# Performance work log

Hardware: AMD Instinct MI355X
Metric: run time of the kernel (lower is better)

## Reference

```python
import jax, jax.numpy as jnp
import numpy as np

B, N, E, H = 8, 512, 1024, 128   # graphs, nodes, edges, hidden
T = 8                             # num_edge_types
HOPS = 3                          # graph_hops


def setup_inputs() -> dict:
    key = jax.random.key(0)
    ks = jax.random.split(key, 10)
    node_feature = jax.random.normal(ks[0], (B, N, H), dtype=jnp.float32)
    edge_vec = jax.random.randint(ks[1], (B, E), 0, T)  # per-edge type ids
    # sparse incidence matrices (one-hot edge endpoints), as the scipy .A densification does
    src = jax.random.randint(ks[2], (B, E), 0, N)
    tgt = jax.random.randint(ks[3], (B, E), 0, N)
    node2edge = jax.nn.one_hot(src, N, dtype=jnp.float32)                 # [B,E,N]
    edge2node = jnp.swapaxes(jax.nn.one_hot(tgt, N, dtype=jnp.float32), 1, 2)  # [B,N,E]
    s = 0.02  # xavier-ish init scale
    edge_weight_tensor = jax.random.normal(ks[4], (T, H * H), dtype=jnp.float32) * s
    Wz = jax.random.normal(ks[5], (2 * H, H), dtype=jnp.float32) * s
    Wr = jax.random.normal(ks[6], (2 * H, H), dtype=jnp.float32) * s
    Wt = jax.random.normal(ks[7], (2 * H, H), dtype=jnp.float32) * s
    Wf = jax.random.normal(ks[8], (4 * H, H), dtype=jnp.float32) * s
    bf = jnp.zeros((H,), dtype=jnp.float32)
    return {"node_feature": node_feature, "edge_vec": edge_vec,
            "node2edge": node2edge, "edge2node": edge2node,
            "edge_weight_tensor": edge_weight_tensor,
            "Wz": Wz, "Wr": Wr, "Wt": Wt, "Wf": Wf, "bf": bf}


def reference(node_feature, edge_vec, node2edge, edge2node,
              edge_weight_tensor, Wz, Wr, Wt, Wf, bf):
    Hd = node_feature.shape[-1]
    # gather per-edge weight matrices once (edge_vec is constant across hops)
    Wedge = edge_weight_tensor[edge_vec].reshape(edge_vec.shape + (Hd, Hd))  # [B,E,H,H]

    def mp(h, n2e, e2n):
        emb = jnp.einsum('ben,bnh->beh', n2e, h)          # gather node states to edges
        new = jnp.einsum('behd,bed->beh', Wedge, emb)     # per-edge-type matvec
        return jnp.einsum('bne,beh->bnh', e2n, new)       # scatter-aggregate to nodes

    def gru_step(h, a):
        x = jnp.concatenate([h, a], axis=-1)
        z = jax.nn.sigmoid(x @ Wz)
        r = jax.nn.sigmoid(x @ Wr)
        t = jnp.tanh(jnp.concatenate([r * h, a], axis=-1) @ Wt)
        return (1.0 - z) * h + z * t

    h = node_feature
    for _ in range(HOPS):
        bw = mp(h, node2edge, edge2node)
        fw = mp(h, jnp.swapaxes(edge2node, 1, 2), jnp.swapaxes(node2edge, 1, 2))
        # GatedFusion(fw, bw)
        z = jax.nn.sigmoid(jnp.concatenate([fw, bw, fw * bw, fw - bw], axis=-1) @ Wf + bf)
        agg = (1.0 - z) * fw + z * bw
        h = gru_step(h, agg)
    return h
```

## Files before the change

kernel.cpp:

```cpp
#include <hip/hip_runtime.h>

#define Bb 8
#define Nn 512
#define Ee 1024
#define Hh 128
#define Tt 8

__device__ __forceinline__ float sigm(float x){ return 1.0f/(1.0f + __expf(-x)); }
__device__ __forceinline__ float tanh_fast(float x){ return 2.0f/(1.0f + __expf(-2.0f*x)) - 1.0f; }

__device__ __forceinline__ void fma4(float* acc, float4 x, float4 w0, float4 w1, float4 w2, float4 w3){
  acc[0] += x.x*w0.x + x.y*w1.x + x.z*w2.x + x.w*w3.x;
  acc[1] += x.x*w0.y + x.y*w1.y + x.z*w2.y + x.w*w3.y;
  acc[2] += x.x*w0.z + x.y*w1.z + x.z*w2.z + x.w*w3.z;
  acc[3] += x.x*w0.w + x.y*w1.w + x.z*w2.w + x.w*w3.w;
}

__global__ void k_extract(const float4* __restrict__ n2e, const float4* __restrict__ e2n,
                          int* __restrict__ src, int* __restrict__ tgt){
  const int total1 = Bb*Ee*Nn/4;
  for (int i = blockIdx.x*blockDim.x + threadIdx.x; i < total1; i += gridDim.x*blockDim.x){
    float4 v = n2e[i];
    if (v.x!=0.f || v.y!=0.f || v.z!=0.f || v.w!=0.f){
      int base = i*4;
      int row = base >> 9;
      int n   = base & 511;
      if (v.x!=0.f) src[row] = n;
      if (v.y!=0.f) src[row] = n+1;
      if (v.z!=0.f) src[row] = n+2;
      if (v.w!=0.f) src[row] = n+3;
    }
  }
  const int total2 = Bb*Nn*Ee/4;
  for (int i = blockIdx.x*blockDim.x + threadIdx.x; i < total2; i += gridDim.x*blockDim.x){
    float4 v = e2n[i];
    if (v.x!=0.f || v.y!=0.f || v.z!=0.f || v.w!=0.f){
      int base = i*4;
      int row = base >> 10;
      int e   = base & 1023;
      int b = row >> 9, n = row & 511;
      int* tp = tgt + b*Ee;
      if (v.x!=0.f) tp[e]   = n;
      if (v.y!=0.f) tp[e+1] = n;
      if (v.z!=0.f) tp[e+2] = n;
      if (v.w!=0.f) tp[e+3] = n;
    }
  }
}

__global__ void k_transW(const float* __restrict__ W, float* __restrict__ WT){
  int i = blockIdx.x*blockDim.x + threadIdx.x;
  if (i >= Tt*Hh*Hh) return;
  int t = i >> 14;
  int h = (i >> 7) & 127;
  int d = i & 127;
  WT[(t*Hh + d)*Hh + h] = W[i];
}

__global__ void k_sort(const int* __restrict__ ev, int* __restrict__ order, int* __restrict__ offs){
  __shared__ int cnt[Tt], offs_s[Tt+1], pos[Tt];
  int b = blockIdx.x, tid = threadIdx.x;
  if (tid < Tt) cnt[tid] = 0;
  __syncthreads();
  for (int e = tid; e < Ee; e += blockDim.x) atomicAdd(&cnt[ev[b*Ee+e]], 1);
  __syncthreads();
  if (tid == 0){ offs_s[0]=0; for (int t=0;t<Tt;t++) offs_s[t+1]=offs_s[t]+cnt[t]; }
  __syncthreads();
  if (tid < Tt) pos[tid] = offs_s[tid];
  if (tid < Tt+1) offs[b*(Tt+1)+tid] = offs_s[tid];
  __syncthreads();
  for (int e = tid; e < Ee; e += blockDim.x){
    int t = ev[b*Ee+e];
    int p = atomicAdd(&pos[t], 1);
    order[b*Ee + p] = e;
  }
}

__global__ __launch_bounds__(256) void k_edge_mp(
    const float* __restrict__ h, const float* __restrict__ WT,
    const int* __restrict__ order, const int* __restrict__ offs,
    const int* __restrict__ src, const int* __restrict__ tgt,
    float* __restrict__ bw, float* __restrict__ fw)
{
  int x = blockIdx.x;
  int dir = x & 1;
  int bt  = x >> 1;
  int t = bt & 7, b = bt >> 3;
  int beg = offs[b*(Tt+1)+t], end = offs[b*(Tt+1)+t+1];
  int chunk0 = beg + blockIdx.y*32;
  if (chunk0 >= end) return;
  const int* gI = dir ? tgt : src;
  const int* sI = dir ? src : tgt;
  float* out = dir ? fw : bw;

  __shared__ float sEmb[32][Hh];
  __shared__ float sW[64][Hh];
  int tid = threadIdx.x;
  int te = tid >> 5, tc = tid & 31;
  int e0 = te*4, c0 = tc*4;
  const float* WTt = WT + t*Hh*Hh;

  for (int chunk = chunk0; chunk < end; chunk += gridDim.y*32){
    int ne = min(32, end - chunk);
    __syncthreads();
    for (int i = tid; i < 32*Hh; i += 256){
      int e = i >> 7, c = i & 127;
      float v = 0.f;
      if (e < ne){
        int eid = order[b*Ee + chunk + e];
        v = h[(b*Nn + gI[b*Ee + eid])*Hh + c];
      }
      sEmb[e][c] = v;
    }
    float acc[4][4] = {};
    for (int kc = 0; kc < Hh; kc += 64){
      __syncthreads();
      for (int i = tid; i < 64*Hh; i += 256){
        int d = i >> 7, c = i & 127;
        sW[d][c] = WTt[(kc + d)*Hh + c];
      }
      __syncthreads();
      #pragma unroll 4
      for (int k = 0; k < 64; k += 4){
        float4 evv[4], wv[4];
        #pragma unroll
        for (int j=0;j<4;j++) evv[j] = *(const float4*)&sEmb[e0+j][kc+k];
        #pragma unroll
        for (int j=0;j<4;j++) wv[j] = *(const float4*)&sW[k+j][c0];
        #pragma unroll
        for (int je=0;je<4;je++) fma4(acc[je], evv[je], wv[0], wv[1], wv[2], wv[3]);
      }
    }
    #pragma unroll
    for (int je=0;je<4;je++){
      int e = e0 + je;
      if (e < ne){
        int eid = order[b*Ee + chunk + e];
        int node = sI[b*Ee + eid];
        float* op = out + (size_t)(b*Nn + node)*Hh + c0;
        atomicAdd(op+0, acc[je][0]);
        atomicAdd(op+1, acc[je][1]);
        atomicAdd(op+2, acc[je][2]);
        atomicAdd(op+3, acc[je][3]);
      }
    }
  }
}

__global__ __launch_bounds__(256) void k_fuse_gru(
    const float* __restrict__ hin, const float* __restrict__ fw, const float* __restrict__ bw,
    const float* __restrict__ Wf, const float* __restrict__ bfv,
    const float* __restrict__ Wz, const float* __restrict__ Wr, const float* __restrict__ Wt,
    float* __restrict__ hout)
{
  __shared__ float sF[16][Hh];
  __shared__ float sS[16][Hh];
  __shared__ float sH[16][Hh];
  int row0 = blockIdx.x * 16;
  int tid = threadIdx.x;
  for (int i = tid; i < 16*Hh; i += 256){
    int r = i >> 7, c = i & 127;
    sF[r][c] = fw[(size_t)(row0+r)*Hh + c];
    sS[r][c] = bw[(size_t)(row0+r)*Hh + c];
    sH[r][c] = hin[(size_t)(row0+r)*Hh + c];
  }
  __syncthreads();
  int te = tid >> 5, tc = tid & 31;
  int r0 = te*2, c0 = tc*4;

  float a0[4] = {0,0,0,0}, a1[4] = {0,0,0,0};
  #pragma unroll
  for (int sec = 0; sec < 4; ++sec){
    #pragma unroll 4
    for (int k = 0; k < Hh; k += 4){
      float4 fa = *(const float4*)&sF[r0][k];
      float4 fb = *(const float4*)&sF[r0+1][k];
      float4 sa = *(const float4*)&sS[r0][k];
      float4 sb = *(const float4*)&sS[r0+1][k];
      float4 xa, xb;
      if      (sec==0){ xa = fa; xb = fb; }
      else if (sec==1){ xa = sa; xb = sb; }
      else if (sec==2){ xa = make_float4(fa.x*sa.x, fa.y*sa.y, fa.z*sa.z, fa.w*sa.w);
                        xb = make_float4(fb.x*sb.x, fb.y*sb.y, fb.z*sb.z, fb.w*sb.w); }
      else            { xa = make_float4(fa.x-sa.x, fa.y-sa.y, fa.z-sa.z, fa.w-sa.w);
                        xb = make_float4(fb.x-sb.x, fb.y-sb.y, fb.z-sb.z, fb.w-sb.w); }
      const float* wp = Wf + (size_t)(sec*Hh + k)*Hh + c0;
      float4 w0 = *(const float4*)(wp);
      float4 w1 = *(const float4*)(wp + Hh);
      float4 w2 = *(const float4*)(wp + 2*Hh);
      float4 w3 = *(const float4*)(wp + 3*Hh);
      fma4(a0, xa, w0, w1, w2, w3);
      fma4(a1, xb, w0, w1, w2, w3);
    }
  }
  float bfx[4] = { bfv[c0], bfv[c0+1], bfv[c0+2], bfv[c0+3] };
  float ag0[4], ag1[4];
  #pragma unroll
  for (int j=0;j<4;j++){
    float zf0 = sigm(a0[j] + bfx[j]);
    float zf1 = sigm(a1[j] + bfx[j]);
    ag0[j] = (1.0f-zf0)*sF[r0][c0+j]   + zf0*sS[r0][c0+j];
    ag1[j] = (1.0f-zf1)*sF[r0+1][c0+j] + zf1*sS[r0+1][c0+j];
  }
  __syncthreads();
  #pragma unroll
  for (int j=0;j<4;j++){ sF[r0][c0+j] = ag0[j]; sF[r0+1][c0+j] = ag1[j]; }
  __syncthreads();

  float az0[4]={0,0,0,0}, az1[4]={0,0,0,0}, ar0[4]={0,0,0,0}, ar1[4]={0,0,0,0};
  #pragma unroll
  for (int sec = 0; sec < 2; ++sec){
    const float (*X)[Hh] = sec ? sF : sH;
    #pragma unroll 4
    for (int k = 0; k < Hh; k += 4){
      float4 xa = *(const float4*)&X[r0][k];
      float4 xb = *(const float4*)&X[r0+1][k];
      const float* wpz = Wz + (size_t)(sec*Hh + k)*Hh + c0;
      const float* wpr = Wr + (size_t)(sec*Hh + k)*Hh + c0;
      float4 z0 = *(const float4*)(wpz);
      float4 z1 = *(const float4*)(wpz + Hh);
      float4 z2 = *(const float4*)(wpz + 2*Hh);
      float4 z3 = *(const float4*)(wpz + 3*Hh);
      fma4(az0, xa, z0, z1, z2, z3);
      fma4(az1, xb, z0, z1, z2, z3);
      float4 r0v = *(const float4*)(wpr);
      float4 r1v = *(const float4*)(wpr + Hh);
      float4 r2v = *(const float4*)(wpr + 2*Hh);
      float4 r3v = *(const float4*)(wpr + 3*Hh);
      fma4(ar0, xa, r0v, r1v, r2v, r3v);
      fma4(ar1, xb, r0v, r1v, r2v, r3v);
    }
  }
  float zz0[4], zz1[4], rh0[4], rh1[4];
  #pragma unroll
  for (int j=0;j<4;j++){
    zz0[j] = sigm(az0[j]);
    zz1[j] = sigm(az1[j]);
    float rr0 = sigm(ar0[j]);
    float rr1 = sigm(ar1[j]);
    rh0[j] = rr0 * sH[r0][c0+j];
    rh1[j] = rr1 * sH[r0+1][c0+j];
  }
  __syncthreads();
  #pragma unroll
  for (int j=0;j<4;j++){ sS[r0][c0+j] = rh0[j]; sS[r0+1][c0+j] = rh1[j]; }
  __syncthreads();

  float at0[4]={0,0,0,0}, at1[4]={0,0,0,0};
  #pragma unroll
  for (int sec = 0; sec < 2; ++sec){
    const float (*X)[Hh] = sec ? sF : sS;
    #pragma unroll 4
    for (int k = 0; k < Hh; k += 4){
      float4 xa = *(const float4*)&X[r0][k];
      float4 xb = *(const float4*)&X[r0+1][k];
      const float* wp = Wt + (size_t)(sec*Hh + k)*Hh + c0;
      float4 w0 = *(const float4*)(wp);
      float4 w1 = *(const float4*)(wp + Hh);
      float4 w2 = *(const float4*)(wp + 2*Hh);
      float4 w3 = *(const float4*)(wp + 3*Hh);
      fma4(at0, xa, w0, w1, w2, w3);
      fma4(at1, xb, w0, w1, w2, w3);
    }
  }
  #pragma unroll
  for (int j=0;j<4;j++){
    float t0 = tanh_fast(at0[j]);
    float t1 = tanh_fast(at1[j]);
    float h0 = sH[r0][c0+j],   h1v = sH[r0+1][c0+j];
    float o0 = (1.0f-zz0[j])*h0  + zz0[j]*t0;
    float o1 = (1.0f-zz1[j])*h1v + zz1[j]*t1;
    hout[(size_t)(row0+r0)*Hh   + c0+j] = o0;
    hout[(size_t)(row0+r0+1)*Hh + c0+j] = o1;
  }
}

extern "C" void kernel_launch(void* const* d_in, const int* in_sizes, int n_in,
                              void* d_out, int out_size, void* d_ws, size_t ws_size,
                              hipStream_t stream){
  const float* node_feature = (const float*)d_in[0];
  const int*   edge_vec     = (const int*)d_in[1];
  const float* n2e          = (const float*)d_in[2];
  const float* e2n          = (const float*)d_in[3];
  const float* Wtensor      = (const float*)d_in[4];
  const float* Wz           = (const float*)d_in[5];
  const float* Wr           = (const float*)d_in[6];
  const float* Wt           = (const float*)d_in[7];
  const float* Wf           = (const float*)d_in[8];
  const float* bf           = (const float*)d_in[9];
  float* out = (float*)d_out;

  char* p = (char*)d_ws;
  int* src   = (int*)p; p += Bb*Ee*4;
  int* tgt   = (int*)p; p += Bb*Ee*4;
  int* order = (int*)p; p += Bb*Ee*4;
  int* offs  = (int*)p; p += 4096;
  float* WT  = (float*)p; p += (size_t)Tt*Hh*Hh*4;
  float* bwp = (float*)p; p += (size_t)Bb*Nn*Hh*4;
  float* fwp = (float*)p; p += (size_t)Bb*Nn*Hh*4;
  float* h1  = (float*)p; p += (size_t)Bb*Nn*Hh*4;

  k_extract<<<1024, 256, 0, stream>>>((const float4*)n2e, (const float4*)e2n, src, tgt);
  k_transW<<<(Tt*Hh*Hh + 255)/256, 256, 0, stream>>>(Wtensor, WT);
  k_sort<<<Bb, 256, 0, stream>>>(edge_vec, order, offs);

  const float* hin = node_feature;
  float* houts[3] = { out, h1, out };
  for (int hop = 0; hop < 3; ++hop){
    hipMemsetAsync(bwp, 0, (size_t)2*Bb*Nn*Hh*4, stream);
    k_edge_mp<<<dim3(Bb*Tt*2, 4), 256, 0, stream>>>(hin, WT, order, offs, src, tgt, bwp, fwp);
    k_fuse_gru<<<(Bb*Nn)/16, 256, 0, stream>>>(hin, fwp, bwp, Wf, bf, Wz, Wr, Wt, houts[hop]);
    hin = houts[hop];
  }
}
```

Before: 536.0 us.

## Stage GRU/fusion weights through double-buffered LDS chunks with 512 threads

```diff
diff --git a/kernel.cpp b/kernel.cpp
--- a/kernel.cpp
+++ b/kernel.cpp
@@ -5,6 +5,9 @@
 #define Ee 1024
 #define Hh 128
 #define Tt 8
+
+#define FG_ROWS 16
+#define FG_PAD 132
 
 __device__ __forceinline__ float sigm(float x){ return 1.0f/(1.0f + __expf(-x)); }
 __device__ __forceinline__ float tanh_fast(float x){ return 2.0f/(1.0f + __expf(-2.0f*x)) - 1.0f; }
@@ -147,132 +150,168 @@
   }
 }
 
-__global__ __launch_bounds__(256) void k_fuse_gru(
+
+#define CK 32
+#define NS 40
+
+__device__ __forceinline__ const float* chunk_ptr(int s, const float* Wf, const float* Wz,
+                                                  const float* Wr, const float* Wt){
+  if (s < 16) return Wf + s*CK*Hh;
+  if (s < 24) return Wz + (s-16)*CK*Hh;
+  if (s < 32) return Wr + (s-24)*CK*Hh;
+  return Wt + (s-32)*CK*Hh;
+}
+
+__device__ __forceinline__ void load_chunk(const float* __restrict__ g, int tid, float4* pf){
+  #pragma unroll
+  for (int it = 0; it < 2; ++it)
+    pf[it] = *(const float4*)(g + (((it<<9) + tid) << 2));
+}
+__device__ __forceinline__ void write_chunk(float* lds, int tid, const float4* pf){
+  #pragma unroll
+  for (int it = 0; it < 2; ++it)
+    *(float4*)(lds + (((it<<9) + tid) << 2)) = pf[it];
+}
+
+__device__ __forceinline__ void chunk_gemm(const float (*X)[FG_PAD], int r, int kb,
+                                           const float (*W)[Hh], int col0, float* acc){
+  #pragma unroll
+  for (int k = 0; k < CK; k += 4){
+    float4 x  = *(const float4*)&X[r][kb+k];
+    float4 w0 = *(const float4*)&W[k+0][col0];
+    float4 w1 = *(const float4*)&W[k+1][col0];
+    float4 w2 = *(const float4*)&W[k+2][col0];
+    float4 w3 = *(const float4*)&W[k+3][col0];
+    fma4(acc, x, w0, w1, w2, w3);
+  }
+}
+
+__device__ __forceinline__ void chunk_gemm_fuse(const float (*A)[FG_PAD], const float (*B)[FG_PAD],
+                                                int mode, int r, int kb, const float (*W)[Hh],
+                                                int col0, float* acc){
+  #pragma unroll
+  for (int k = 0; k < CK; k += 4){
+    float4 a = *(const float4*)&A[r][kb+k];
+    float4 b = *(const float4*)&B[r][kb+k];
+    float4 x;
+    if (mode == 0) x = make_float4(a.x*b.x, a.y*b.y, a.z*b.z, a.w*b.w);
+    else           x = make_float4(a.x-b.x, a.y-b.y, a.z-b.z, a.w-b.w);
+    float4 w0 = *(const float4*)&W[k+0][col0];
+    float4 w1 = *(const float4*)&W[k+1][col0];
+    float4 w2 = *(const float4*)&W[k+2][col0];
+    float4 w3 = *(const float4*)&W[k+3][col0];
+    fma4(acc, x, w0, w1, w2, w3);
+  }
+}
+
+__global__ __launch_bounds__(512) void k_fuse_gru(
     const float* __restrict__ hin, const float* __restrict__ fw, const float* __restrict__ bw,
     const float* __restrict__ Wf, const float* __restrict__ bfv,
     const float* __restrict__ Wz, const float* __restrict__ Wr, const float* __restrict__ Wt,
     float* __restrict__ hout)
 {
-  __shared__ float sF[16][Hh];
-  __shared__ float sS[16][Hh];
-  __shared__ float sH[16][Hh];
-  int row0 = blockIdx.x * 16;
-  int tid = threadIdx.x;
-  for (int i = tid; i < 16*Hh; i += 256){
-    int r = i >> 7, c = i & 127;
-    sF[r][c] = fw[(size_t)(row0+r)*Hh + c];
-    sS[r][c] = bw[(size_t)(row0+r)*Hh + c];
-    sH[r][c] = hin[(size_t)(row0+r)*Hh + c];
-  }
-  __syncthreads();
-  int te = tid >> 5, tc = tid & 31;
-  int r0 = te*2, c0 = tc*4;
-
-  float a0[4] = {0,0,0,0}, a1[4] = {0,0,0,0};
-  #pragma unroll
-  for (int sec = 0; sec < 4; ++sec){
-    #pragma unroll 4
-    for (int k = 0; k < Hh; k += 4){
-      float4 fa = *(const float4*)&sF[r0][k];
-      float4 fb = *(const float4*)&sF[r0+1][k];
-      float4 sa = *(const float4*)&sS[r0][k];
-      float4 sb = *(const float4*)&sS[r0+1][k];
-      float4 xa, xb;
-      if      (sec==0){ xa = fa; xb = fb; }
-      else if (sec==1){ xa = sa; xb = sb; }
-      else if (sec==2){ xa = make_float4(fa.x*sa.x, fa.y*sa.y, fa.z*sa.z, fa.w*sa.w);
-                        xb = make_float4(fb.x*sb.x, fb.y*sb.y, fb.z*sb.z, fb.w*sb.w); }
-      else            { xa = make_float4(fa.x-sa.x, fa.y-sa.y, fa.z-sa.z, fa.w-sa.w);
-                        xb = make_float4(fb.x-sb.x, fb.y-sb.y, fb.z-sb.z, fb.w-sb.w); }
-      const float* wp = Wf + (size_t)(sec*Hh + k)*Hh + c0;
-      float4 w0 = *(const float4*)(wp);
-      float4 w1 = *(const float4*)(wp + Hh);
-      float4 w2 = *(const float4*)(wp + 2*Hh);
-      float4 w3 = *(const float4*)(wp + 3*Hh);
-      fma4(a0, xa, w0, w1, w2, w3);
-      fma4(a1, xb, w0, w1, w2, w3);
-    }
-  }
-  float bfx[4] = { bfv[c0], bfv[c0+1], bfv[c0+2], bfv[c0+3] };
-  float ag0[4], ag1[4];
-  #pragma unroll
-  for (int j=0;j<4;j++){
-    float zf0 = sigm(a0[j] + bfx[j]);
-    float zf1 = sigm(a1[j] + bfx[j]);
-    ag0[j] = (1.0f-zf0)*sF[r0][c0+j]   + zf0*sS[r0][c0+j];
-    ag1[j] = (1.0f-zf1)*sF[r0+1][c0+j] + zf1*sS[r0+1][c0+j];
-  }
-  __syncthreads();
-  #pragma unroll
-  for (int j=0;j<4;j++){ sF[r0][c0+j] = ag0[j]; sF[r0+1][c0+j] = ag1[j]; }
-  __syncthreads();
-
-  float az0[4]={0,0,0,0}, az1[4]={0,0,0,0}, ar0[4]={0,0,0,0}, ar1[4]={0,0,0,0};
-  #pragma unroll
-  for (int sec = 0; sec < 2; ++sec){
-    const float (*X)[Hh] = sec ? sF : sH;
-    #pragma unroll 4
-    for (int k = 0; k < Hh; k += 4){
-      float4 xa = *(const float4*)&X[r0][k];
-      float4 xb = *(const float4*)&X[r0+1][k];
-      const float* wpz = Wz + (size_t)(sec*Hh + k)*Hh + c0;
-      const float* wpr = Wr + (size_t)(sec*Hh + k)*Hh + c0;
-      float4 z0 = *(const float4*)(wpz);
-      float4 z1 = *(const float4*)(wpz + Hh);
-      float4 z2 = *(const float4*)(wpz + 2*Hh);
-      float4 z3 = *(const float4*)(wpz + 3*Hh);
-      fma4(az0, xa, z0, z1, z2, z3);
-      fma4(az1, xb, z0, z1, z2, z3);
-      float4 r0v = *(const float4*)(wpr);
-      float4 r1v = *(const float4*)(wpr + Hh);
-      float4 r2v = *(const float4*)(wpr + 2*Hh);
-      float4 r3v = *(const float4*)(wpr + 3*Hh);
-      fma4(ar0, xa, r0v, r1v, r2v, r3v);
-      fma4(ar1, xb, r0v, r1v, r2v, r3v);
-    }
-  }
-  float zz0[4], zz1[4], rh0[4], rh1[4];
-  #pragma unroll
-  for (int j=0;j<4;j++){
-    zz0[j] = sigm(az0[j]);
-    zz1[j] = sigm(az1[j]);
-    float rr0 = sigm(ar0[j]);
-    float rr1 = sigm(ar1[j]);
-    rh0[j] = rr0 * sH[r0][c0+j];
-    rh1[j] = rr1 * sH[r0+1][c0+j];
-  }
-  __syncthreads();
-  #pragma unroll
-  for (int j=0;j<4;j++){ sS[r0][c0+j] = rh0[j]; sS[r0+1][c0+j] = rh1[j]; }
-  __syncthreads();
-
-  float at0[4]={0,0,0,0}, at1[4]={0,0,0,0};
-  #pragma unroll
-  for (int sec = 0; sec < 2; ++sec){
-    const float (*X)[Hh] = sec ? sF : sS;
-    #pragma unroll 4
-    for (int k = 0; k < Hh; k += 4){
-      float4 xa = *(const float4*)&X[r0][k];
-      float4 xb = *(const float4*)&X[r0+1][k];
-      const float* wp = Wt + (size_t)(sec*Hh + k)*Hh + c0;
-      float4 w0 = *(const float4*)(wp);
-      float4 w1 = *(const float4*)(wp + Hh);
-      float4 w2 = *(const float4*)(wp + 2*Hh);
-      float4 w3 = *(const float4*)(wp + 3*Hh);
-      fma4(at0, xa, w0, w1, w2, w3);
-      fma4(at1, xb, w0, w1, w2, w3);
-    }
-  }
-  #pragma unroll
-  for (int j=0;j<4;j++){
-    float t0 = tanh_fast(at0[j]);
-    float t1 = tanh_fast(at1[j]);
-    float h0 = sH[r0][c0+j],   h1v = sH[r0+1][c0+j];
-    float o0 = (1.0f-zz0[j])*h0  + zz0[j]*t0;
-    float o1 = (1.0f-zz1[j])*h1v + zz1[j]*t1;
-    hout[(size_t)(row0+r0)*Hh   + c0+j] = o0;
-    hout[(size_t)(row0+r0+1)*Hh + c0+j] = o1;
-  }
+  __shared__ float sF[FG_ROWS][FG_PAD];
+  __shared__ float sS[FG_ROWS][FG_PAD];
+  __shared__ float sH[FG_ROWS][FG_PAD];
+  __shared__ float sW[2][CK][Hh];
+
+  int tid  = threadIdx.x;
+  int row0 = blockIdx.x * FG_ROWS;
+  int lane = tid & 63, w = tid >> 6;
+  int r    = lane >> 2;
+  int col0 = w*16 + (lane & 3)*4;
+
+  float4 pf[2];
+  load_chunk(chunk_ptr(0, Wf, Wz, Wr, Wt), tid, pf);
+
+  {
+    int ir = tid >> 5;
+    int k0 = (tid & 31) << 2;
+    size_t gofs = (size_t)(row0 + ir)*Hh + k0;
+    float4 fv = *(const float4*)&fw[gofs];
+    float4 bv = *(const float4*)&bw[gofs];
+    float4 hv = *(const float4*)&hin[gofs];
+    *(float4*)&sF[ir][k0] = fv;
+    *(float4*)&sS[ir][k0] = bv;
+    *(float4*)&sH[ir][k0] = hv;
+  }
+  float4 bias4 = *(const float4*)&bfv[col0];
+
+  write_chunk(&sW[0][0][0], tid, pf);
+  load_chunk(chunk_ptr(1, Wf, Wz, Wr, Wt), tid, pf);
+  __syncthreads();
+
+  float af[4] = {0,0,0,0};
+  for (int s = 0; s < 16; ++s){
+    const float (*Wb)[Hh] = (const float (*)[Hh])sW[s&1];
+    int sec = s >> 2, kb = (s & 3)*CK;
+    if      (sec == 0) chunk_gemm(sF, r, kb, Wb, col0, af);
+    else if (sec == 1) chunk_gemm(sS, r, kb, Wb, col0, af);
+    else if (sec == 2) chunk_gemm_fuse(sF, sS, 0, r, kb, Wb, col0, af);
+    else               chunk_gemm_fuse(sF, sS, 1, r, kb, Wb, col0, af);
+    write_chunk(&sW[(s+1)&1][0][0], tid, pf);
+    load_chunk(chunk_ptr(s+2, Wf, Wz, Wr, Wt), tid, pf);
+    __syncthreads();
+  }
+
+  float agv[4];
+  {
+    float bb[4] = {bias4.x, bias4.y, bias4.z, bias4.w};
+    #pragma unroll
+    for (int j = 0; j < 4; ++j){
+      float z = sigm(af[j] + bb[j]);
+      agv[j] = (1.0f - z)*sF[r][col0+j] + z*sS[r][col0+j];
+    }
+  }
+  *(float4*)&sF[r][col0] = make_float4(agv[0], agv[1], agv[2], agv[3]);
+  __syncthreads();
+
+  float az[4] = {0,0,0,0}, ar[4] = {0,0,0,0};
+  for (int s = 16; s < 32; ++s){
+    const float (*Wb)[Hh] = (const float (*)[Hh])sW[s&1];
+    int q = s - 16;
+    int kb = (q & 3)*CK;
+    const float (*X)[FG_PAD] = ((q & 4) ? sF : sH);
+    if (q < 8) chunk_gemm(X, r, kb, Wb, col0, az);
+    else       chunk_gemm(X, r, kb, Wb, col0, ar);
+    write_chunk(&sW[(s+1)&1][0][0], tid, pf);
+    load_chunk(chunk_ptr(s+2, Wf, Wz, Wr, Wt), tid, pf);
+    __syncthreads();
+  }
+
+  float zz[4];
+  {
+    float rh[4];
+    #pragma unroll
+    for (int j = 0; j < 4; ++j){
+      zz[j] = sigm(az[j]);
+      rh[j] = sigm(ar[j]) * sH[r][col0+j];
+    }
+    *(float4*)&sS[r][col0] = make_float4(rh[0], rh[1], rh[2], rh[3]);
+  }
+  __syncthreads();
+
+  float at[4] = {0,0,0,0};
+  for (int s = 32; s < NS; ++s){
+    const float (*Wb)[Hh] = (const float (*)[Hh])sW[s&1];
+    int q = s - 32;
+    int kb = (q & 3)*CK;
+    const float (*X)[FG_PAD] = ((q & 4) ? sF : sS);
+    chunk_gemm(X, r, kb, Wb, col0, at);
+    if (s < NS-1){
+      write_chunk(&sW[(s+1)&1][0][0], tid, pf);
+      if (s < NS-2) load_chunk(chunk_ptr(s+2, Wf, Wz, Wr, Wt), tid, pf);
+      __syncthreads();
+    }
+  }
+
+  float o[4];
+  #pragma unroll
+  for (int j = 0; j < 4; ++j){
+    float t = tanh_fast(at[j]);
+    o[j] = (1.0f - zz[j])*sH[r][col0+j] + zz[j]*t;
+  }
+  *(float4*)&hout[(size_t)(row0 + r)*Hh + col0] = make_float4(o[0], o[1], o[2], o[3]);
 }
 
 extern "C" void kernel_launch(void* const* d_in, const int* in_sizes, int n_in,
@@ -309,7 +348,7 @@
   for (int hop = 0; hop < 3; ++hop){
     hipMemsetAsync(bwp, 0, (size_t)2*Bb*Nn*Hh*4, stream);
     k_edge_mp<<<dim3(Bb*Tt*2, 4), 256, 0, stream>>>(hin, WT, order, offs, src, tgt, bwp, fwp);
-    k_fuse_gru<<<(Bb*Nn)/16, 256, 0, stream>>>(hin, fwp, bwp, Wf, bf, Wz, Wr, Wt, houts[hop]);
+    k_fuse_gru<<<(Bb*Nn)/FG_ROWS, 512, 0, stream>>>(hin, fwp, bwp, Wf, bf, Wz, Wr, Wt, houts[hop]);
     hin = houts[hop];
   }
 }
```

Result: faster. 477.8 us (-10.9%).
